# Optimization experiments

Hardware: AMD Instinct MI355X
Metric: run time of the kernel (lower is better)

## Reference

```python
import jax, jax.numpy as jnp
import numpy as np

EPS = 1e-12


def conv3(x, W, b):
    # x: [B,C,H,W], W: [O,I,3,3] -> SAME conv, stride 1
    y = jax.lax.conv_general_dilated(x, W, (1, 1), 'SAME',
                                     dimension_numbers=('NCHW', 'OIHW', 'NCHW'))
    return y + b[None, :, None, None]


def unfold3(x):
    # torch F.unfold(kernel=3, padding=1): [B,C,H,W] -> [B, C*9, H*W]
    B, C, H, W = x.shape
    xp = jnp.pad(x, ((0, 0), (0, 0), (1, 1), (1, 1)))
    patches = jnp.stack([xp[:, :, i:i + H, j:j + W]
                         for i in range(3) for j in range(3)], axis=2)  # [B,C,9,H,W]
    return patches.reshape(B, C * 9, H * W)


def fold3(u, H, W):
    # torch F.fold(kernel=3, padding=1): [B, C*9, H*W] -> [B,C,H,W] (overlap-add)
    B = u.shape[0]
    C = u.shape[1] // 9
    p = u.reshape(B, C, 3, 3, H, W)
    out = jnp.zeros((B, C, H + 2, W + 2), u.dtype)
    for i in range(3):
        for j in range(3):
            out = out.at[:, :, i:i + H, j:j + W].add(p[:, :, i, j])
    return out[:, :, 1:-1, 1:-1]


def l2norm(v, axis):
    n = jnp.sqrt(jnp.sum(v * v, axis=axis, keepdims=True))
    return v / jnp.maximum(n, EPS)


def setup_inputs() -> dict:
    key = jax.random.key(0)
    ks = jax.random.split(key, 10)
    in_c, q_c = 64, 32
    B, H, W = 1, 96, 96
    s = 0.05
    return {
        'x':  jax.random.normal(ks[0], (B, in_c, H, W), jnp.float32),
        'W1': jax.random.normal(ks[1], (in_c, in_c, 3, 3), jnp.float32) * s,
        'b1': jax.random.normal(ks[2], (in_c,), jnp.float32) * s,
        'W2': jax.random.normal(ks[3], (in_c, in_c, 3, 3), jnp.float32) * s,
        'b2': jax.random.normal(ks[4], (in_c,), jnp.float32) * s,
        'Wq': jax.random.normal(ks[5], (q_c, in_c, 3, 3), jnp.float32) * s,
        'bq': jax.random.normal(ks[6], (q_c,), jnp.float32) * s,
        'Wk': jax.random.normal(ks[7], (q_c, in_c, 3, 3), jnp.float32) * s,
        'bk': jax.random.normal(ks[8], (q_c,), jnp.float32) * s,
    }


def reference(x, W1, b1, W2, b2, Wq, bq, Wk, bk):
    TOPK = 5
    B, C, H, W = x.shape
    L = H * W

    feature = jax.nn.relu(conv3(jax.nn.relu(conv3(x, W1, b1)), W2, b2))
    q = conv3(x, Wq, bq)
    k = conv3(x, Wk, bk)

    q_unfold = l2norm(unfold3(q), axis=1)                      # [B, Q9, L]
    k_unfold = l2norm(jnp.swapaxes(unfold3(k), 1, 2), axis=2)  # [B, L, Q9]

    R_qk = jnp.einsum('blc,bcm->blm', k_unfold, q_unfold)      # [B, L_k, L_q]

    # topk over dim=1 (key positions) for each query position
    vals, idxs = jax.lax.top_k(jnp.swapaxes(R_qk, 1, 2), TOPK)  # [B, L_q, K]
    R_maxs = jnp.swapaxes(vals, 1, 2)                           # [B, K, L]
    R_indexs = jnp.swapaxes(idxs, 1, 2)                         # [B, K, L]

    x_unfold = unfold3(x)                                       # [B, C*9, L]
    acc = jnp.zeros_like(x)
    for i in range(1, TOPK):
        idx = R_indexs[:, i, :][:, None, :]                     # [B,1,L]
        T_unfold = jnp.take_along_axis(x_unfold, idx, axis=2)   # [B, C*9, L]
        T = fold3(T_unfold, H, W) / 9.0
        S = R_maxs[:, i, :].reshape(B, 1, H, W)
        acc = acc + T * S
    y = feature + x + acc / float(TOPK - 1)
    return y
```

## Files before the change

kernel.cpp:

```cpp
#include <hip/hip_runtime.h>
#include <math.h>

#define HH 96
#define WW 96
#define LL 9216
#define D9 288
#define TOPK 5
#define NK 6
#define NCAND 8
#define KSPLIT 32
#define CPQ (KSPLIT * NK)
#define KEYS_PER_SPLIT (LL / KSPLIT)
#define PASSES (KEYS_PER_SPLIT / 32)
#define CHUNKS (32 * 36)
#define KROW 292

typedef short short8 __attribute__((ext_vector_type(8)));
typedef float f32x16 __attribute__((ext_vector_type(16)));

__device__ __forceinline__ float  asf(unsigned u) { union { unsigned u; float f; } a; a.u = u; return a.f; }
__device__ __forceinline__ unsigned asu(float f)  { union { float f; unsigned u; } a; a.f = f; return a.u; }

__device__ __forceinline__ unsigned short f2bf(float f) {
    unsigned u = asu(f);
    unsigned r = u + 0x7fff + ((u >> 16) & 1);
    return (unsigned short)(r >> 16);
}

template<int N>
__device__ __forceinline__ void ins_med3(float* v, float x) {
    float nv[N];
    nv[0] = fmaxf(v[0], x);
    #pragma unroll
    for (int s = 1; s < N; ++s) nv[s] = __builtin_amdgcn_fmed3f(v[s-1], v[s], x);
    #pragma unroll
    for (int s = 0; s < N; ++s) v[s] = nv[s];
}

__device__ __forceinline__ bool better_tb(float av, int ai, float bv, int bi) {
    return (av > bv) || (av == bv && ai < bi);
}

template<int N>
__device__ __forceinline__ void insert_tb(float (&v)[N], int (&ix)[N], float nv, int ni) {
    if (better_tb(nv, ni, v[N-1], ix[N-1])) {
        v[N-1] = nv; ix[N-1] = ni;
        #pragma unroll
        for (int s = N-1; s > 0; --s) {
            if (better_tb(v[s], ix[s], v[s-1], ix[s-1])) {
                float tv = v[s]; v[s] = v[s-1]; v[s-1] = tv;
                int ti = ix[s]; ix[s] = ix[s-1]; ix[s-1] = ti;
            }
        }
    }
}

__global__ __launch_bounds__(256) void conv_stage1_kernel(
    const float* __restrict__ x,
    const float* __restrict__ W1, const float* __restrict__ b1, float* __restrict__ c1,
    const float* __restrict__ Wq, const float* __restrict__ bq,
    const float* __restrict__ Wk, const float* __restrict__ bk,
    float* __restrict__ qq, float* __restrict__ kk)
{
    int pix = blockIdx.x * 256 + threadIdx.x;
    int y = pix / WW, x0 = pix % WW;

    int  offs[9]; bool msk[9];
    #pragma unroll
    for (int u = 0; u < 3; ++u)
        #pragma unroll
        for (int v = 0; v < 3; ++v) {
            int yy = y + u - 1, xx = x0 + v - 1;
            bool ok = ((unsigned)yy < 96u) && ((unsigned)xx < 96u);
            msk[u*3+v]  = ok;
            offs[u*3+v] = ok ? (yy*96 + xx) : 0;
        }

    int g = blockIdx.y;
    if (g < 16) {
        int co0 = g * 4;
        float acc[4];
        #pragma unroll
        for (int j = 0; j < 4; ++j) acc[j] = b1[co0 + j];
        #pragma unroll 2
        for (int ci = 0; ci < 64; ++ci) {
            const float* xp = x + (size_t)ci * LL;
            float v9[9];
            #pragma unroll
            for (int t = 0; t < 9; ++t) v9[t] = msk[t] ? xp[offs[t]] : 0.0f;
            const float* wb = W1 + ((size_t)co0 * 64 + ci) * 9;
            #pragma unroll
            for (int j = 0; j < 4; ++j) {
                const float* wp = wb + (size_t)j * 64 * 9;
                #pragma unroll
                for (int t = 0; t < 9; ++t) acc[j] = fmaf(v9[t], wp[t], acc[j]);
            }
        }
        #pragma unroll
        for (int j = 0; j < 4; ++j)
            c1[(size_t)(co0 + j) * LL + pix] = fmaxf(acc[j], 0.0f);
    } else {
        int co0 = (g - 16) * 4;
        float aq[4], ak[4];
        #pragma unroll
        for (int j = 0; j < 4; ++j) { aq[j] = bq[co0 + j]; ak[j] = bk[co0 + j]; }
        #pragma unroll 2
        for (int ci = 0; ci < 64; ++ci) {
            const float* xp = x + (size_t)ci * LL;
            float v9[9];
            #pragma unroll
            for (int t = 0; t < 9; ++t) v9[t] = msk[t] ? xp[offs[t]] : 0.0f;
            #pragma unroll
            for (int j = 0; j < 4; ++j) {
                const float* wpq = Wq + ((size_t)(co0 + j) * 64 + ci) * 9;
                const float* wpk = Wk + ((size_t)(co0 + j) * 64 + ci) * 9;
                #pragma unroll
                for (int t = 0; t < 9; ++t) {
                    aq[j] = fmaf(v9[t], wpq[t], aq[j]);
                    ak[j] = fmaf(v9[t], wpk[t], ak[j]);
                }
            }
        }
        #pragma unroll
        for (int j = 0; j < 4; ++j) {
            qq[(size_t)(co0 + j) * LL + pix] = aq[j];
            kk[(size_t)(co0 + j) * LL + pix] = ak[j];
        }
    }
}

__global__ __launch_bounds__(256) void conv3_co4_kernel(
    const float* __restrict__ in, const float* __restrict__ Wt,
    const float* __restrict__ bias, float* __restrict__ out)
{
    int co0 = blockIdx.y * 4;
    int pix = blockIdx.x * 256 + threadIdx.x;
    int y = pix / WW, x = pix % WW;

    int  offs[9]; bool msk[9];
    #pragma unroll
    for (int u = 0; u < 3; ++u)
        #pragma unroll
        for (int v = 0; v < 3; ++v) {
            int yy = y + u - 1, xx = x + v - 1;
            bool ok = ((unsigned)yy < 96u) && ((unsigned)xx < 96u);
            msk[u*3+v]  = ok;
            offs[u*3+v] = ok ? (yy*96 + xx) : 0;
        }

    float acc[4];
    #pragma unroll
    for (int j = 0; j < 4; ++j) acc[j] = bias[co0 + j];

    #pragma unroll 2
    for (int ci = 0; ci < 64; ++ci) {
        const float* xp = in + (size_t)ci * LL;
        float v9[9];
        #pragma unroll
        for (int t = 0; t < 9; ++t) v9[t] = msk[t] ? xp[offs[t]] : 0.0f;
        const float* wb = Wt + ((size_t)co0 * 64 + ci) * 9;
        #pragma unroll
        for (int j = 0; j < 4; ++j) {
            const float* wp = wb + (size_t)j * 64 * 9;
            #pragma unroll
            for (int t = 0; t < 9; ++t) acc[j] = fmaf(v9[t], wp[t], acc[j]);
        }
    }
    #pragma unroll
    for (int j = 0; j < 4; ++j)
        out[(size_t)(co0 + j) * LL + pix] = fmaxf(acc[j], 0.0f);
}

__global__ __launch_bounds__(256) void transpose_x_kernel(
    const float* __restrict__ x, float* __restrict__ xT)
{
    __shared__ float t[64][65];
    int pix0 = blockIdx.x * 64;
    int lp = threadIdx.x & 63, cg = threadIdx.x >> 6;
    #pragma unroll
    for (int cc = 0; cc < 16; ++cc) {
        int c = cg * 16 + cc;
        t[c][lp] = x[(size_t)c * LL + pix0 + lp];
    }
    __syncthreads();
    #pragma unroll
    for (int pp = 0; pp < 16; ++pp) {
        int pl = cg * 16 + pp;
        xT[(size_t)(pix0 + pl) * 64 + lp] = t[lp][pl];
    }
}

__global__ __launch_bounds__(256) void unfold_norm_kernel(
    const float* __restrict__ qq, float* __restrict__ q_f32, unsigned short* __restrict__ q_bf,
    const float* __restrict__ kk, float* __restrict__ k_f32, unsigned short* __restrict__ k_bf)
{
    const float* in; float* o32; unsigned short* obf;
    if (blockIdx.y == 0) { in = qq; o32 = q_f32; obf = q_bf; }
    else                 { in = kk; o32 = k_f32; obf = k_bf; }

    __shared__ float tile[3][32][34];
    __shared__ float inv_s[32];
    int tid = threadIdx.x;
    int l0 = blockIdx.x * 32;
    int y = l0 / WW, xb = l0 % WW;

    #pragma unroll
    for (int j = 0; j < 13; ++j) {
        int f = j * 256 + tid;
        if (f < 3 * 32 * 34) {
            int col = f % 34, cc = (f / 34) & 31, r = f / (34 * 32);
            int yy = y + r - 1, xv = xb + col - 1;
            float val = ((unsigned)yy < 96u && (unsigned)xv < 96u)
                        ? in[(size_t)cc * LL + yy * 96 + xv] : 0.0f;
            tile[r][cc][col] = val;
        }
    }
    __syncthreads();

    {
        int pxl = tid >> 3, sub = tid & 7;
        float ss = 0.0f;
        #pragma unroll
        for (int cc = 0; cc < 4; ++cc) {
            int c = sub * 4 + cc;
            #pragma unroll
            for (int u = 0; u < 3; ++u)
                #pragma unroll
                for (int v = 0; v < 3; ++v) {
                    float val = tile[u][c][pxl + v];
                    ss = fmaf(val, val, ss);
                }
        }
        ss += __shfl_xor(ss, 1);
        ss += __shfl_xor(ss, 2);
        ss += __shfl_xor(ss, 4);
        if (sub == 0) inv_s[pxl] = 1.0f / fmaxf(sqrtf(ss), 1e-12f);
    }
    __syncthreads();

    #pragma unroll 1
    for (int it = 0; it < 9; ++it) {
        int e = it * 256 + tid;
        int pxl = e / 72, dc = e - pxl * 72;
        int l = l0 + pxl;
        float inv = inv_s[pxl];
        float4 o; float* op = &o.x;
        #pragma unroll
        for (int i = 0; i < 4; ++i) {
            int d = dc * 4 + i;
            int c = d / 9, rm = d - c * 9;
            int u = rm / 3, v = rm - u * 3;
            op[i] = tile[u][c][pxl + v] * inv;
        }
        *(float4*)(o32 + (size_t)l * D9 + dc * 4) = o;
        unsigned short b4[4];
        #pragma unroll
        for (int i = 0; i < 4; ++i) b4[i] = f2bf(op[i]);
        *(uint2*)(obf + (size_t)l * D9 + dc * 4) = *(uint2*)b4;
    }
}

__global__ __launch_bounds__(256, 2) void topk_mfma_kernel(
    const unsigned short* __restrict__ qn_bf, const unsigned short* __restrict__ kn_bf,
    float* __restrict__ valsQ)
{
    __shared__ unsigned short ks[2][32 * KROW];

    int tid  = threadIdx.x;
    int lane = tid & 63;
    int col = lane & 31, khalf = lane >> 5;
    int qtile = blockIdx.x >> 5;
    int split = blockIdx.x & 31;
    int q0w = qtile * 256 + (tid >> 6) * 64;
    int key0 = split * KEYS_PER_SPLIT;

    short8 qf[2][18];
    #pragma unroll
    for (int b = 0; b < 2; ++b) {
        const unsigned short* qrow = qn_bf + (size_t)(q0w + b*32 + col) * D9 + khalf * 8;
        #pragma unroll
        for (int dg = 0; dg < 18; ++dg)
            qf[b][dg] = *(const short8*)(qrow + dg * 16);
    }

    float lv0[NK], lv1[NK];
    #pragma unroll
    for (int s = 0; s < NK; ++s) { lv0[s] = -INFINITY; lv1[s] = -INFINITY; }

    const char* kg = (const char*)kn_bf;
    uint4 pre[5];

    #pragma unroll
    for (int c0 = 0; c0 < 5; ++c0) {
        int c = tid + c0 * 256;
        if (c < CHUNKS) {
            int key = c / 36, off = c - key * 36;
            pre[c0] = *(const uint4*)(kg + (size_t)(key0 + key) * 576 + off * 16);
        }
    }
    #pragma unroll
    for (int c0 = 0; c0 < 5; ++c0) {
        int c = tid + c0 * 256;
        if (c < CHUNKS) {
            int key = c / 36, off = c - key * 36;
            char* d = (char*)ks[0] + key * (KROW*2) + off * 16;
            *(uint2*)d       = *(uint2*)&pre[c0];
            *(uint2*)(d + 8) = *((uint2*)&pre[c0] + 1);
        }
    }
    __syncthreads();

    for (int p = 0; p < PASSES; ++p) {
        if (p + 1 < PASSES) {
            #pragma unroll
            for (int c0 = 0; c0 < 5; ++c0) {
                int c = tid + c0 * 256;
                if (c < CHUNKS) {
                    int key = c / 36, off = c - key * 36;
                    pre[c0] = *(const uint4*)(kg + (size_t)(key0 + (p+1)*32 + key) * 576 + off * 16);
                }
            }
        }

        f32x16 acc0 = {}, acc1 = {};
        const char* kb = (const char*)ks[p & 1] + (size_t)col * (KROW*2) + khalf * 16;
        #pragma unroll
        for (int dg = 0; dg < 18; ++dg) {
            short8 af;
            *(uint2*)&af       = *(const uint2*)(kb + dg * 32);
            *((uint2*)&af + 1) = *(const uint2*)(kb + dg * 32 + 8);
            acc0 = __builtin_amdgcn_mfma_f32_32x32x16_bf16(af, qf[0][dg], acc0, 0, 0, 0);
            acc1 = __builtin_amdgcn_mfma_f32_32x32x16_bf16(af, qf[1][dg], acc1, 0, 0, 0);
        }

        int lbase = p * 32 + 4 * khalf;
        #pragma unroll
        for (int r = 0; r < 16; ++r) {
            unsigned lkey = (unsigned)(lbase + (r & 3) + 8 * (r >> 2));
            ins_med3<NK>(lv0, asf((asu(acc0[r]) & 0xFFFFFE00u) | lkey));
            ins_med3<NK>(lv1, asf((asu(acc1[r]) & 0xFFFFFE00u) | lkey));
        }

        if (p + 1 < PASSES) {
            #pragma unroll
            for (int c0 = 0; c0 < 5; ++c0) {
                int c = tid + c0 * 256;
                if (c < CHUNKS) {
                    int key = c / 36, off = c - key * 36;
                    char* d = (char*)ks[(p+1) & 1] + key * (KROW*2) + off * 16;
                    *(uint2*)d       = *(uint2*)&pre[c0];
                    *(uint2*)(d + 8) = *((uint2*)&pre[c0] + 1);
                }
            }
        }
        __syncthreads();
    }

    #pragma unroll
    for (int b = 0; b < 2; ++b) {
        float* lv = b ? lv1 : lv0;
        float pv[NK];
        #pragma unroll
        for (int s = 0; s < NK; ++s) pv[s] = __shfl_xor(lv[s], 32);
        #pragma unroll
        for (int s = 0; s < NK; ++s) ins_med3<NK>(lv, pv[s]);
        if (lane < 32) {
            int q = q0w + b * 32 + col;
            float* vq = valsQ + (size_t)q * CPQ + split * NK;
            #pragma unroll
            for (int s = 0; s < NK; ++s) vq[s] = lv[s];
        }
    }
}

__global__ __launch_bounds__(256) void rerank_kernel(
    const float* __restrict__ valsQ,
    const float* __restrict__ qn_f32, const float* __restrict__ kn_f32,
    float* __restrict__ vals, int* __restrict__ idxs)
{
    int tid = threadIdx.x;
    int lane = tid & 63;
    int half = lane >> 5, l32 = lane & 31;
    int q = blockIdx.x * 8 + (tid >> 6) * 2 + half;

    const float* vq = valsQ + (size_t)q * CPQ + l32 * NK;
    float v[NK];
    #pragma unroll
    for (int s = 0; s < NK; ++s) v[s] = vq[s];

    int ckey[NCAND];
    #pragma unroll
    for (int it = 0; it < NCAND; ++it) {
        float cv = v[0];
        int cl = l32;
        #pragma unroll
        for (int st = 1; st < 32; st <<= 1) {
            float ov = __shfl_xor(cv, st);
            int ol = __shfl_xor(cl, st);
            if (ov > cv || (ov == cv && ol < cl)) { cv = ov; cl = ol; }
        }
        ckey[it] = cl * KEYS_PER_SPLIT + (int)(asu(cv) & 0x1FFu);
        if (cl == l32) {
            #pragma unroll
            for (int s = 0; s < NK-1; ++s) v[s] = v[s+1];
            v[NK-1] = -INFINITY;
        }
    }

    int r = l32 >> 2, part = l32 & 3;
    const float4* qr = (const float4*)(qn_f32 + (size_t)q * D9) + part * 18;
    const float4* kr = (const float4*)(kn_f32 + (size_t)ckey[r] * D9) + part * 18;
    float s0 = 0.f, s1 = 0.f, s2 = 0.f, s3 = 0.f;
    #pragma unroll
    for (int i2 = 0; i2 < 18; ++i2) {
        float4 a = qr[i2], b = kr[i2];
        s0 = fmaf(a.x, b.x, s0); s1 = fmaf(a.y, b.y, s1);
        s2 = fmaf(a.z, b.z, s2); s3 = fmaf(a.w, b.w, s3);
    }
    float sc = (s0 + s1) + (s2 + s3);
    sc += __shfl_xor(sc, 1);
    sc += __shfl_xor(sc, 2);

    float bv[TOPK]; int bi[TOPK];
    #pragma unroll
    for (int s = 0; s < TOPK; ++s) { bv[s] = -INFINITY; bi[s] = 0x7fffffff; }
    #pragma unroll
    for (int cc = 0; cc < NCAND; ++cc) {
        float sv = __shfl(sc, half * 32 + cc * 4);
        insert_tb<TOPK>(bv, bi, sv, ckey[cc]);
    }
    if (l32 == 0) {
        #pragma unroll
        for (int s = 0; s < TOPK; ++s) {
            vals[(size_t)s * LL + q] = bv[s];
            idxs[(size_t)s * LL + q] = bi[s];
        }
    }
}

__global__ __launch_bounds__(256) void gather_out_kernel(
    const float* __restrict__ xT, const float* __restrict__ feat,
    const float* __restrict__ vals, const int* __restrict__ idxs,
    float* __restrict__ out)
{
    int wave = threadIdx.x >> 6, lane = threadIdx.x & 63;
    int pix = blockIdx.x * 4 + wave;
    int y = pix / WW, x0 = pix - y * WW;
    float acc = 0.0f;
    #pragma unroll 1
    for (int s = 1; s < TOPK; ++s) {
        float S = vals[(size_t)s * LL + pix] * (1.0f/9.0f);
        #pragma unroll
        for (int i = 0; i < 3; ++i) {
            int qy = y + 1 - i;
            #pragma unroll
            for (int j = 0; j < 3; ++j) {
                int qx = x0 + 1 - j;
                if ((unsigned)qy < 96u && (unsigned)qx < 96u) {
                    int l = idxs[(size_t)s * LL + qy * WW + qx];
                    int yl = l / WW, xl = l - yl * WW;
                    int sy = yl + i - 1, sx = xl + j - 1;
                    if ((unsigned)sy < 96u && (unsigned)sx < 96u)
                        acc = fmaf(S, xT[(size_t)(sy * WW + sx) * 64 + lane], acc);
                }
            }
        }
    }
    out[(size_t)lane * LL + pix] = feat[(size_t)lane * LL + pix]
                                 + xT[(size_t)pix * 64 + lane] + acc * 0.25f;
}

extern "C" void kernel_launch(void* const* d_in, const int* in_sizes, int n_in,
                              void* d_out, int out_size, void* d_ws, size_t ws_size,
                              hipStream_t stream)
{
    (void)in_sizes; (void)n_in; (void)out_size; (void)ws_size;
    const float* x  = (const float*)d_in[0];
    const float* W1 = (const float*)d_in[1];
    const float* b1 = (const float*)d_in[2];
    const float* W2 = (const float*)d_in[3];
    const float* b2 = (const float*)d_in[4];
    const float* Wq = (const float*)d_in[5];
    const float* bq = (const float*)d_in[6];
    const float* Wk = (const float*)d_in[7];
    const float* bk = (const float*)d_in[8];
    float* out = (float*)d_out;

    char* p = (char*)d_ws;
    float* c1     = (float*)p;            p += (size_t)64 * LL * 4;
    float* feat   = (float*)p;            p += (size_t)64 * LL * 4;
    float* xT     = (float*)p;            p += (size_t)64 * LL * 4;
    float* qq     = (float*)p;            p += (size_t)32 * LL * 4;
    float* kk     = (float*)p;            p += (size_t)32 * LL * 4;
    float* qn_f32 = (float*)p;            p += (size_t)LL * D9 * 4;
    float* kn_f32 = (float*)p;            p += (size_t)LL * D9 * 4;
    unsigned short* qn_bf = (unsigned short*)p;  p += (size_t)LL * D9 * 2;
    unsigned short* kn_bf = (unsigned short*)p;  p += (size_t)LL * D9 * 2;
    float* valsQ  = (float*)p;            p += (size_t)LL * CPQ * 4;
    float* vals   = (float*)p;            p += (size_t)TOPK * LL * 4;
    int*   idxs   = (int*)p;              p += (size_t)TOPK * LL * 4;

    conv_stage1_kernel<<<dim3(36, 24), 256, 0, stream>>>(x, W1, b1, c1, Wq, bq, Wk, bk, qq, kk);
    unfold_norm_kernel<<<dim3(288, 2), 256, 0, stream>>>(qq, qn_f32, qn_bf, kk, kn_f32, kn_bf);
    topk_mfma_kernel<<<36 * KSPLIT, 256, 0, stream>>>(qn_bf, kn_bf, valsQ);
    conv3_co4_kernel<<<dim3(36, 16), 256, 0, stream>>>(c1, W2, b2, feat);
    transpose_x_kernel<<<144, 256, 0, stream>>>(x, xT);
    rerank_kernel<<<LL / 8, 256, 0, stream>>>(valsQ, qn_f32, kn_f32, vals, idxs);
    gather_out_kernel<<<LL / 4, 256, 0, stream>>>(xT, feat, vals, idxs, out);
}
```

Baseline: 307.2 us.

## Stage conv input tiles in LDS and compute eight output channels per thread

```diff
diff --git a/kernel.cpp b/kernel.cpp
--- a/kernel.cpp
+++ b/kernel.cpp
@@ -55,6 +55,61 @@
     }
 }
 
+__device__ __forceinline__ void conv8_staged(
+    const float* __restrict__ in, const float* __restrict__ Wt,
+    const float* __restrict__ bias, float* __restrict__ out,
+    int co0, int doRelu, float* lds)
+{
+    int tid = threadIdx.x;
+    int pix = blockIdx.x * 256 + tid;
+    int p_row = pix / WW, p_col = pix - p_row * WW;
+    int r_lo = (blockIdx.x * 256) / WW;
+    int rbase = p_row - r_lo + 1;
+
+    float acc[8];
+    #pragma unroll
+    for (int j = 0; j < 8; ++j) acc[j] = bias[co0 + j];
+
+    #pragma unroll 1
+    for (int chunk = 0; chunk < 4; ++chunk) {
+        int ci0 = chunk * 16;
+        #pragma unroll
+        for (int s = 0; s < 36; ++s) {
+            int flat = s * 256 + tid;
+            int seg = flat / 96, col = flat - seg * 96;
+            int g_r = r_lo - 1 + (seg >> 4);
+            int ci  = ci0 + (seg & 15);
+            float val = ((unsigned)g_r < 96u) ? in[(size_t)ci * LL + g_r * WW + col] : 0.0f;
+            lds[seg * 100 + col + 1] = val;
+        }
+        if (tid < 192) lds[(tid >> 1) * 100 + ((tid & 1) ? 97 : 0)] = 0.0f;
+        __syncthreads();
+
+        #pragma unroll 2
+        for (int ci = 0; ci < 16; ++ci) {
+            float v9[9];
+            #pragma unroll
+            for (int u = 0; u < 3; ++u)
+                #pragma unroll
+                for (int v = 0; v < 3; ++v)
+                    v9[u*3+v] = lds[((rbase + u - 1) * 16 + ci) * 100 + p_col + v];
+            const float* wb = Wt + ((size_t)co0 * 64 + (ci0 + ci)) * 9;
+            #pragma unroll
+            for (int j = 0; j < 8; ++j) {
+                const float* wp = wb + (size_t)j * 64 * 9;
+                #pragma unroll
+                for (int t = 0; t < 9; ++t) acc[j] = fmaf(v9[t], wp[t], acc[j]);
+            }
+        }
+        __syncthreads();
+    }
+    #pragma unroll
+    for (int j = 0; j < 8; ++j) {
+        float r = doRelu ? fmaxf(acc[j], 0.0f) : acc[j];
+        out[(size_t)(co0 + j) * LL + pix] = r;
+    }
+}
+
 __global__ __launch_bounds__(256) void conv_stage1_kernel(
     const float* __restrict__ x,
     const float* __restrict__ W1, const float* __restrict__ b1, float* __restrict__ c1,
@@ -62,113 +117,19 @@
     const float* __restrict__ Wk, const float* __restrict__ bk,
     float* __restrict__ qq, float* __restrict__ kk)
 {
-    int pix = blockIdx.x * 256 + threadIdx.x;
-    int y = pix / WW, x0 = pix % WW;
-
-    int  offs[9]; bool msk[9];
-    #pragma unroll
-    for (int u = 0; u < 3; ++u)
-        #pragma unroll
-        for (int v = 0; v < 3; ++v) {
-            int yy = y + u - 1, xx = x0 + v - 1;
-            bool ok = ((unsigned)yy < 96u) && ((unsigned)xx < 96u);
-            msk[u*3+v]  = ok;
-            offs[u*3+v] = ok ? (yy*96 + xx) : 0;
-        }
-
+    __shared__ float lds[6 * 16 * 100];
     int g = blockIdx.y;
-    if (g < 16) {
-        int co0 = g * 4;
-        float acc[4];
-        #pragma unroll
-        for (int j = 0; j < 4; ++j) acc[j] = b1[co0 + j];
-        #pragma unroll 2
-        for (int ci = 0; ci < 64; ++ci) {
-            const float* xp = x + (size_t)ci * LL;
-            float v9[9];
-            #pragma unroll
-            for (int t = 0; t < 9; ++t) v9[t] = msk[t] ? xp[offs[t]] : 0.0f;
-            const float* wb = W1 + ((size_t)co0 * 64 + ci) * 9;
-            #pragma unroll
-            for (int j = 0; j < 4; ++j) {
-                const float* wp = wb + (size_t)j * 64 * 9;
-                #pragma unroll
-                for (int t = 0; t < 9; ++t) acc[j] = fmaf(v9[t], wp[t], acc[j]);
-            }
-        }
-        #pragma unroll
-        for (int j = 0; j < 4; ++j)
-            c1[(size_t)(co0 + j) * LL + pix] = fmaxf(acc[j], 0.0f);
-    } else {
-        int co0 = (g - 16) * 4;
-        float aq[4], ak[4];
-        #pragma unroll
-        for (int j = 0; j < 4; ++j) { aq[j] = bq[co0 + j]; ak[j] = bk[co0 + j]; }
-        #pragma unroll 2
-        for (int ci = 0; ci < 64; ++ci) {
-            const float* xp = x + (size_t)ci * LL;
-            float v9[9];
-            #pragma unroll
-            for (int t = 0; t < 9; ++t) v9[t] = msk[t] ? xp[offs[t]] : 0.0f;
-            #pragma unroll
-            for (int j = 0; j < 4; ++j) {
-                const float* wpq = Wq + ((size_t)(co0 + j) * 64 + ci) * 9;
-                const float* wpk = Wk + ((size_t)(co0 + j) * 64 + ci) * 9;
-                #pragma unroll
-                for (int t = 0; t < 9; ++t) {
-                    aq[j] = fmaf(v9[t], wpq[t], aq[j]);
-                    ak[j] = fmaf(v9[t], wpk[t], ak[j]);
-                }
-            }
-        }
-        #pragma unroll
-        for (int j = 0; j < 4; ++j) {
-            qq[(size_t)(co0 + j) * LL + pix] = aq[j];
-            kk[(size_t)(co0 + j) * LL + pix] = ak[j];
-        }
-    }
-}
-
-__global__ __launch_bounds__(256) void conv3_co4_kernel(
-    const float* __restrict__ in, const float* __restrict__ Wt,
-    const float* __restrict__ bias, float* __restrict__ out)
-{
-    int co0 = blockIdx.y * 4;
-    int pix = blockIdx.x * 256 + threadIdx.x;
-    int y = pix / WW, x = pix % WW;
-
-    int  offs[9]; bool msk[9];
-    #pragma unroll
-    for (int u = 0; u < 3; ++u)
-        #pragma unroll
-        for (int v = 0; v < 3; ++v) {
-            int yy = y + u - 1, xx = x + v - 1;
-            bool ok = ((unsigned)yy < 96u) && ((unsigned)xx < 96u);
-            msk[u*3+v]  = ok;
-            offs[u*3+v] = ok ? (yy*96 + xx) : 0;
-        }
-
-    float acc[4];
-    #pragma unroll
-    for (int j = 0; j < 4; ++j) acc[j] = bias[co0 + j];
-
-    #pragma unroll 2
-    for (int ci = 0; ci < 64; ++ci) {
-        const float* xp = in + (size_t)ci * LL;
-        float v9[9];
-        #pragma unroll
-        for (int t = 0; t < 9; ++t) v9[t] = msk[t] ? xp[offs[t]] : 0.0f;
-        const float* wb = Wt + ((size_t)co0 * 64 + ci) * 9;
-        #pragma unroll
-        for (int j = 0; j < 4; ++j) {
-            const float* wp = wb + (size_t)j * 64 * 9;
-            #pragma unroll
-            for (int t = 0; t < 9; ++t) acc[j] = fmaf(v9[t], wp[t], acc[j]);
-        }
-    }
-    #pragma unroll
-    for (int j = 0; j < 4; ++j)
-        out[(size_t)(co0 + j) * LL + pix] = fmaxf(acc[j], 0.0f);
+    if (g < 8)       conv8_staged(x, W1, b1, c1, g * 8,        1, lds);
+    else if (g < 12) conv8_staged(x, Wq, bq, qq, (g - 8) * 8,  0, lds);
+    else             conv8_staged(x, Wk, bk, kk, (g - 12) * 8, 0, lds);
+}
+
+__global__ __launch_bounds__(256) void conv2_kernel(
+    const float* __restrict__ c1, const float* __restrict__ W2,
+    const float* __restrict__ b2, float* __restrict__ feat)
+{
+    __shared__ float lds[6 * 16 * 100];
+    conv8_staged(c1, W2, b2, feat, blockIdx.y * 8, 1, lds);
 }
 
 __global__ __launch_bounds__(256) void transpose_x_kernel(
@@ -500,10 +461,10 @@
     float* vals   = (float*)p;            p += (size_t)TOPK * LL * 4;
     int*   idxs   = (int*)p;              p += (size_t)TOPK * LL * 4;
 
-    conv_stage1_kernel<<<dim3(36, 24), 256, 0, stream>>>(x, W1, b1, c1, Wq, bq, Wk, bk, qq, kk);
+    conv_stage1_kernel<<<dim3(36, 16), 256, 0, stream>>>(x, W1, b1, c1, Wq, bq, Wk, bk, qq, kk);
     unfold_norm_kernel<<<dim3(288, 2), 256, 0, stream>>>(qq, qn_f32, qn_bf, kk, kn_f32, kn_bf);
     topk_mfma_kernel<<<36 * KSPLIT, 256, 0, stream>>>(qn_bf, kn_bf, valsQ);
-    conv3_co4_kernel<<<dim3(36, 16), 256, 0, stream>>>(c1, W2, b2, feat);
+    conv2_kernel<<<dim3(36, 8), 256, 0, stream>>>(c1, W2, b2, feat);
     transpose_x_kernel<<<144, 256, 0, stream>>>(x, xT);
     rerank_kernel<<<LL / 8, 256, 0, stream>>>(valsQ, qn_f32, kn_f32, vals, idxs);
     gather_out_kernel<<<LL / 4, 256, 0, stream>>>(xT, feat, vals, idxs, out);
```

New measurement: 379.7 us. 1.24x slower.
